# Optimization experiments

Measured on AMD Instinct MI355X. Metric: run time of the kernel, lower is better.

## Reference

```python
import jax, jax.numpy as jnp
import numpy as np

B, L, M = 512, 128, 6
ATOM_DIM, BOND_DIM, FP = 39, 10, 256


def setup_inputs() -> dict:
    key = jax.random.key(0)
    ks = jax.random.split(key, 16)
    s = 0.05
    inp = {
        'atom_list': jax.random.normal(ks[0], (B, L, ATOM_DIM), jnp.float32),
        'bond_list': jax.random.normal(ks[1], (B, L, BOND_DIM), jnp.float32),
        'atom_degree_list': jax.random.randint(ks[2], (B, L, M), 0, L),
        'bond_degree_list': jax.random.randint(ks[3], (B, L, M), 0, L),
        'atom_mask': jnp.ones((B, L), jnp.float32),
        # parameters (torch Linear convention: W [out, in], y = x @ W.T + b)
        'W_atom': jax.random.normal(ks[4], (FP, ATOM_DIM), jnp.float32) * s,
        'b_atom': jnp.zeros((FP,), jnp.float32),
        'W_nbr': jax.random.normal(ks[5], (FP, ATOM_DIM + BOND_DIM), jnp.float32) * s,
        'b_nbr': jnp.zeros((FP,), jnp.float32),
        'W_align': jax.random.normal(ks[6], (1, 2 * FP), jnp.float32) * s,
        'b_align': jnp.zeros((1,), jnp.float32),
        'W_attend': jax.random.normal(ks[7], (FP, FP), jnp.float32) * s,
        'b_attend': jnp.zeros((FP,), jnp.float32),
        # GRUCell params, gate order (r, z, n)
        'W_ih': jax.random.normal(ks[8], (3 * FP, FP), jnp.float32) * s,
        'b_ih': jnp.zeros((3 * FP,), jnp.float32),
        'W_hh': jax.random.normal(ks[9], (3 * FP, FP), jnp.float32) * s,
        'b_hh': jnp.zeros((3 * FP,), jnp.float32),
    }
    return inp


def _leaky(x):
    return jax.nn.leaky_relu(x, negative_slope=0.01)


def _gru_cell(x, h, W_ih, b_ih, W_hh, b_hh):
    gi = x @ W_ih.T + b_ih  # [N, 3F]
    gh = h @ W_hh.T + b_hh
    i_r, i_z, i_n = jnp.split(gi, 3, axis=-1)
    h_r, h_z, h_n = jnp.split(gh, 3, axis=-1)
    r = jax.nn.sigmoid(i_r + h_r)
    z = jax.nn.sigmoid(i_z + h_z)
    n = jnp.tanh(i_n + r * h_n)
    return (1.0 - z) * n + z * h


def reference(atom_list, bond_list, atom_degree_list, bond_degree_list, atom_mask,
              W_atom, b_atom, W_nbr, b_nbr, W_align, b_align, W_attend, b_attend,
              W_ih, b_ih, W_hh, b_hh):
    batch, mol_length, _ = atom_list.shape
    bidx = jnp.arange(batch)[:, None, None]

    atom_feature = _leaky(atom_list @ W_atom.T + b_atom)  # [B,L,F]

    # per-molecule neighbor gathers (irregular access)
    atom_neighbor = atom_list[bidx, atom_degree_list]   # [B,L,M,ATOM_DIM]
    bond_neighbor = bond_list[bidx, bond_degree_list]   # [B,L,M,BOND_DIM]
    neighbor_feature = jnp.concatenate([atom_neighbor, bond_neighbor], axis=-1)
    neighbor_feature = _leaky(neighbor_feature @ W_nbr.T + b_nbr)  # [B,L,M,F]

    pad = atom_degree_list == (mol_length - 1)
    attend_mask = jnp.where(pad, 0.0, 1.0)[..., None]          # [B,L,M,1]
    softmax_mask = jnp.where(pad, -9e8, 0.0)[..., None]        # [B,L,M,1]

    atom_feature_expand = jnp.broadcast_to(atom_feature[:, :, None, :],
                                           neighbor_feature.shape)
    feature_align = jnp.concatenate([atom_feature_expand, neighbor_feature], axis=-1)
    align_score = _leaky(feature_align @ W_align.T + b_align)  # [B,L,M,1]
    align_score = align_score + softmax_mask
    attention_weight = jax.nn.softmax(align_score, axis=-2) * attend_mask

    neighbor_transform = neighbor_feature @ W_attend.T + b_attend  # [B,L,M,F]
    context = jnp.sum(attention_weight * neighbor_transform, axis=-2)  # [B,L,F]
    context = jax.nn.elu(context)

    h = _gru_cell(context.reshape(-1, context.shape[-1]),
                  atom_feature.reshape(-1, atom_feature.shape[-1]),
                  W_ih, b_ih, W_hh, b_hh)
    atom_feature = h.reshape(batch, mol_length, -1)
    return jax.nn.relu(atom_feature)
```

## Files before the change

### kernel.cpp

```cpp
#include <hip/hip_runtime.h>
#include <hip/hip_bf16.h>
#include <math.h>

#define Bsz 512
#define Lm  128
#define Mn  6
#define AD  39
#define BDm 10
#define KN  49
#define F   256
#define TB  16
#define NR  96
#define NFP 264
#define ANP 72

#define WS_WATM 0
#define WS_WNBR 32768
#define WS_WATT 65536
#define WS_WIH  196608
#define WS_WHH  589824
#define WS_WALN 983040
#define WS_SUM  991232
#define WS_WN   1253376

typedef __attribute__((ext_vector_type(8))) short bf16x8;
typedef __attribute__((ext_vector_type(4))) float f32x4;
typedef __attribute__((ext_vector_type(4))) unsigned int u32x4;

__device__ __forceinline__ float lrelu(float x){ return x > 0.0f ? x : 0.01f*x; }
__device__ __forceinline__ float sigm(float x){ return 1.0f/(1.0f+__expf(-x)); }
__device__ __forceinline__ float ftanh(float x){
    float xc = fminf(fmaxf(x, -15.f), 15.f);
    float e  = __expf(2.0f*xc);
    return (e - 1.0f)/(e + 1.0f);
}
__device__ __forceinline__ float felu(float x){ return x > 0.f ? x : (__expf(x) - 1.0f); }

__device__ __forceinline__ unsigned short f2bfh(float f){
    __hip_bfloat16 h = __float2bfloat16(f);
    unsigned short s;
    __builtin_memcpy(&s, &h, 2);
    return s;
}
__device__ __forceinline__ unsigned int pack2bf(float lo, float hi){
    float2 f2; f2.x = lo; f2.y = hi;
    __hip_bfloat162 h2 = __float22bfloat162_rn(f2);
    unsigned int u;
    __builtin_memcpy(&u, &h2, 4);
    return u;
}
__device__ __forceinline__ float bf2f(unsigned short h){
    unsigned int u = ((unsigned int)h)<<16;
    return __builtin_bit_cast(float, u);
}

__global__ __launch_bounds__(256)
void p0_prep(const float* __restrict__ Watm, const float* __restrict__ Wnbr,
             const float* __restrict__ Watt, const float* __restrict__ Wih,
             const float* __restrict__ Whh,  const float* __restrict__ Waln,
             unsigned short* __restrict__ ws)
{
    int id = blockIdx.x*256 + threadIdx.x;
    if (id >= 968*512) return;
    int T = id >> 9, e = id & 511;
    int lane = e >> 3, j = e & 7;
    int col16 = lane & 15, kg = lane >> 4;
    float v; unsigned short* dst;
    if (T < 32) {
        int nt = T >> 1, ks = T & 1;
        int k = ks*32 + kg*8 + j;
        v = (k < AD) ? Watm[(nt*16 + col16)*AD + k] : 0.0f;
        dst = ws + (WS_WATM>>1) + (size_t)T*512 + e;
    } else if (T < 64) {
        int T2 = T - 32;
        int nt = T2 >> 1, ks = T2 & 1;
        int k = ks*32 + kg*8 + j;
        v = (k < KN) ? Wnbr[(nt*16 + col16)*KN + k] : 0.0f;
        dst = ws + (WS_WNBR>>1) + (size_t)T2*512 + e;
    } else if (T < 192) {
        int T2 = T - 64;
        int nt = T2 >> 3, ks = T2 & 7;
        v = Watt[(nt*16 + col16)*F + ks*32 + kg*8 + j];
        dst = ws + (WS_WATT>>1) + (size_t)T2*512 + e;
    } else if (T < 576) {
        int T3 = T - 192;
        int nt = T3 >> 3, ks = T3 & 7;
        v = Wih[(nt*16 + col16)*F + ks*32 + kg*8 + j];
        dst = ws + (WS_WIH>>1) + (size_t)T3*512 + e;
    } else if (T < 960) {
        int T4 = T - 576;
        int nt = T4 >> 3, ks = T4 & 7;
        v = Whh[(nt*16 + col16)*F + ks*32 + kg*8 + j];
        dst = ws + (WS_WHH>>1) + (size_t)T4*512 + e;
    } else {
        int ks = T - 960;
        v = (col16 == 0) ? Waln[F + ks*32 + kg*8 + j] : 0.0f;
        dst = ws + (WS_WALN>>1) + (size_t)ks*512 + e;
    }
    *dst = f2bfh(v);
}

#define NT2 512
__global__ __launch_bounds__(NT2, 6)
void k2_nbr(const float* __restrict__ atom, const float* __restrict__ bond,
            const int* __restrict__ adeg_g, const int* __restrict__ bdeg_g,
            const float* __restrict__ Walign, const float* __restrict__ balign,
            const float* __restrict__ batom,  const float* __restrict__ bnbr,
            const unsigned short* __restrict__ ws,
            unsigned short* __restrict__ wn_g, float* __restrict__ sumaw_g)
{
    __shared__ alignas(16) unsigned short nfl[NR*NFP];
    __shared__ float ascl[TB];
    __shared__ float nscl[NR];
    __shared__ float awl[NR];
    __shared__ int   adeg[NR];
    __shared__ int   bdeg[NR];
    unsigned short* stg = nfl;

    const int t  = threadIdx.x;
    const int g0 = blockIdx.x*TB;
    const int molbase = (g0/Lm)*Lm;
    const int w = t >> 6, lane = t & 63;
    const int col16 = lane & 15, kg = lane >> 4;

    bf16x8 batmf[2][2], bnbrf[2][2];
    #pragma unroll
    for (int j = 0; j < 2; ++j)
        #pragma unroll
        for (int ks = 0; ks < 2; ++ks) {
            batmf[j][ks] = *(const bf16x8*)&ws[(WS_WATM>>1) + (size_t)((2*w+j)*2 + ks)*512 + lane*8];
            bnbrf[j][ks] = *(const bf16x8*)&ws[(WS_WNBR>>1) + (size_t)((2*w+j)*2 + ks)*512 + lane*8];
        }

    if (t < NR) {
        adeg[t] = adeg_g[(size_t)g0*Mn + t];
        bdeg[t] = bdeg_g[(size_t)g0*Mn + t];
    }
    if (t < TB) ascl[t] = 0.f;
    __syncthreads();

    for (int i = t; i < 112*32; i += NT2) {
        int r = i >> 5, d0 = (i & 31)*2;
        float v0, v1;
        if (r < TB) {
            const float* src = atom + (size_t)(g0+r)*AD;
            v0 = (d0   < AD) ? src[d0]   : 0.f;
            v1 = (d0+1 < AD) ? src[d0+1] : 0.f;
        } else {
            int rr = r - TB;
            const float* asrc = atom + (size_t)(molbase + adeg[rr])*AD;
            const float* bsrc = bond + (size_t)(molbase + bdeg[rr])*BDm;
            int d1 = d0+1;
            v0 = (d0 < AD) ? asrc[d0] : ((d0 < KN) ? bsrc[d0-AD] : 0.f);
            v1 = (d1 < AD) ? asrc[d1] : ((d1 < KN) ? bsrc[d1-AD] : 0.f);
        }
        *(unsigned int*)&stg[r*ANP + d0] = pack2bf(v0, v1);
    }
    __syncthreads();

    {
        f32x4 acc[2];
        #pragma unroll
        for (int j = 0; j < 2; ++j) acc[j] = (f32x4){0.f,0.f,0.f,0.f};
        #pragma unroll
        for (int ks = 0; ks < 2; ++ks) {
            bf16x8 a = *(const bf16x8*)&stg[col16*ANP + ks*32 + kg*8];
            #pragma unroll
            for (int j = 0; j < 2; ++j)
                acc[j] = __builtin_amdgcn_mfma_f32_16x16x32_bf16(a, batmf[j][ks], acc[j], 0, 0, 0);
        }
        float ps[4] = {0.f,0.f,0.f,0.f};
        #pragma unroll
        for (int j = 0; j < 2; ++j) {
            const int col = (2*w+j)*16 + col16;
            const float bb  = batom[col];
            const float wal = Walign[col];
            #pragma unroll
            for (int jj = 0; jj < 4; ++jj) ps[jj] += lrelu(acc[j][jj] + bb)*wal;
        }
        #pragma unroll
        for (int jj = 0; jj < 4; ++jj) {
            float p = ps[jj];
            p += __shfl_xor(p, 1); p += __shfl_xor(p, 2);
            p += __shfl_xor(p, 4); p += __shfl_xor(p, 8);
            if (col16 == 0) atomicAdd(&ascl[kg*4 + jj], p);
        }
    }

    f32x4 acc[6][2];
    #pragma unroll
    for (int mt = 0; mt < 6; ++mt)
        #pragma unroll
        for (int j = 0; j < 2; ++j) acc[mt][j] = (f32x4){0.f,0.f,0.f,0.f};
    #pragma unroll
    for (int ks = 0; ks < 2; ++ks) {
        #pragma unroll
        for (int mt = 0; mt < 6; ++mt) {
            bf16x8 a = *(const bf16x8*)&stg[(TB + mt*16 + col16)*ANP + ks*32 + kg*8];
            #pragma unroll
            for (int j = 0; j < 2; ++j)
                acc[mt][j] = __builtin_amdgcn_mfma_f32_16x16x32_bf16(a, bnbrf[j][ks], acc[mt][j], 0, 0, 0);
        }
    }
    __syncthreads();

    #pragma unroll
    for (int mt = 0; mt < 6; ++mt)
        #pragma unroll
        for (int j = 0; j < 2; ++j) {
            const int col = (2*w+j)*16 + col16;
            const float bnb = bnbr[col];
            #pragma unroll
            for (int jj = 0; jj < 4; ++jj)
                nfl[(mt*16 + kg*4 + jj)*NFP + col] = f2bfh(lrelu(acc[mt][j][jj] + bnb));
        }
    __syncthreads();

    if (w < 6) {
        const int mt = w;
        f32x4 ns = {0.f,0.f,0.f,0.f};
        #pragma unroll
        for (int ks = 0; ks < 8; ++ks) {
            bf16x8 a = *(const bf16x8*)&nfl[(mt*16 + col16)*NFP + ks*32 + kg*8];
            bf16x8 b = *(const bf16x8*)&ws[(WS_WALN>>1) + (size_t)ks*512 + lane*8];
            ns = __builtin_amdgcn_mfma_f32_16x16x32_bf16(a, b, ns, 0, 0, 0);
        }
        if (col16 == 0) {
            #pragma unroll
            for (int jj = 0; jj < 4; ++jj) nscl[mt*16 + kg*4 + jj] = ns[jj];
        }
    }
    __syncthreads();

    if (t < TB) {
        const float ba = balign[0];
        const float as = ascl[t];
        float sc[Mn], msk[Mn];
        float mx = -1e30f;
        #pragma unroll
        for (int m = 0; m < Mn; ++m) {
            int pad = (adeg[t*Mn+m] == Lm-1);
            float s = lrelu(as + nscl[t*Mn+m] + ba) + (pad ? -9e8f : 0.0f);
            msk[m] = pad ? 0.f : 1.f;
            sc[m] = s; mx = fmaxf(mx, s);
        }
        float sum = 0.f;
        #pragma unroll
        for (int m = 0; m < Mn; ++m) { sc[m] = __expf(sc[m]-mx); sum += sc[m]; }
        const float inv = 1.0f/sum;
        float sa = 0.f;
        #pragma unroll
        for (int m = 0; m < Mn; ++m) { float v = sc[m]*inv*msk[m]; awl[t*Mn+m] = v; sa += v; }
        sumaw_g[g0 + t] = sa;
    }
    __syncthreads();

    {
        const int a = t & 15, cg = t >> 4;
        float o[8] = {0,0,0,0,0,0,0,0};
        #pragma unroll
        for (int m = 0; m < Mn; ++m) {
            const float aw = awl[a*Mn + m];
            u32x4 v = *(const u32x4*)&nfl[(a*Mn+m)*NFP + cg*8];
            o[0] += aw*__builtin_bit_cast(float, v.x<<16);
            o[1] += aw*__builtin_bit_cast(float, v.x & 0xffff0000u);
            o[2] += aw*__builtin_bit_cast(float, v.y<<16);
            o[3] += aw*__builtin_bit_cast(float, v.y & 0xffff0000u);
            o[4] += aw*__builtin_bit_cast(float, v.z<<16);
            o[5] += aw*__builtin_bit_cast(float, v.z & 0xffff0000u);
            o[6] += aw*__builtin_bit_cast(float, v.w<<16);
            o[7] += aw*__builtin_bit_cast(float, v.w & 0xffff0000u);
        }
        u32x4 pv;
        pv.x = pack2bf(o[0], o[1]);
        pv.y = pack2bf(o[2], o[3]);
        pv.z = pack2bf(o[4], o[5]);
        pv.w = pack2bf(o[6], o[7]);
        __builtin_nontemporal_store(pv, (u32x4*)&wn_g[(size_t)(g0+a)*F + cg*8]);
    }
}

#define NTK4 512
#define K4A  64
__global__ __launch_bounds__(NTK4)
void k4_gru(const unsigned short* __restrict__ ws,
            const unsigned short* __restrict__ wn_g,
            const float* __restrict__ atom,
            const float* __restrict__ sumaw_g, const float* __restrict__ batom,
            const float* __restrict__ batt,
            const float* __restrict__ bih, const float* __restrict__ bhh,
            float* __restrict__ out)
{
    __shared__ alignas(16) unsigned short wnl[K4A*NFP];
    __shared__ alignas(16) unsigned short afl[K4A*NFP];
    __shared__ alignas(16) unsigned short arowl[K4A*ANP];
    __shared__ float sumawl[K4A];
    const int t  = threadIdx.x;
    const int g0 = blockIdx.x*K4A;

    for (int i = t; i < K4A*32; i += NTK4) {
        int row = i >> 5, cg = i & 31;
        u32x4 v = __builtin_nontemporal_load((const u32x4*)&wn_g[(size_t)(g0+row)*F + cg*8]);
        *(u32x4*)&wnl[row*NFP + cg*8] = v;
    }
    for (int i = t; i < K4A*32; i += NTK4) {
        int r = i >> 5, d0 = (i & 31)*2;
        const float* src = atom + (size_t)(g0+r)*AD;
        float v0 = (d0   < AD) ? __builtin_nontemporal_load(&src[d0])   : 0.f;
        float v1 = (d0+1 < AD) ? __builtin_nontemporal_load(&src[d0+1]) : 0.f;
        *(unsigned int*)&arowl[r*ANP + d0] = pack2bf(v0, v1);
    }
    if (t < K4A) sumawl[t] = sumaw_g[g0 + t];
    __syncthreads();

    const int w = t >> 6, lane = t & 63;
    const int col16 = lane & 15, kg = lane >> 4;
    const unsigned short* wsAtm = ws + (WS_WATM>>1);
    const unsigned short* wsAtt = ws + (WS_WATT>>1);
    const unsigned short* wsIh  = ws + (WS_WIH>>1);
    const unsigned short* wsHh  = ws + (WS_WHH>>1);

    {
        f32x4 a0[4], a1[4];
        #pragma unroll
        for (int mt = 0; mt < 4; ++mt) { a0[mt] = (f32x4){0,0,0,0}; a1[mt] = (f32x4){0,0,0,0}; }
        #pragma unroll
        for (int ks = 0; ks < 2; ++ks) {
            bf16x8 b0 = *(const bf16x8*)&wsAtm[(size_t)((2*w)*2   + ks)*512 + lane*8];
            bf16x8 b1 = *(const bf16x8*)&wsAtm[(size_t)((2*w+1)*2 + ks)*512 + lane*8];
            #pragma unroll
            for (int mt = 0; mt < 4; ++mt) {
                bf16x8 a = *(const bf16x8*)&arowl[(mt*16 + col16)*ANP + ks*32 + kg*8];
                a0[mt] = __builtin_amdgcn_mfma_f32_16x16x32_bf16(a, b0, a0[mt], 0, 0, 0);
                a1[mt] = __builtin_amdgcn_mfma_f32_16x16x32_bf16(a, b1, a1[mt], 0, 0, 0);
            }
        }
        const float bb0 = batom[(2*w)*16   + col16];
        const float bb1 = batom[(2*w+1)*16 + col16];
        #pragma unroll
        for (int mt = 0; mt < 4; ++mt)
            #pragma unroll
            for (int jj = 0; jj < 4; ++jj) {
                int row = mt*16 + kg*4 + jj;
                afl[row*NFP + (2*w)*16   + col16] = f2bfh(lrelu(a0[mt][jj] + bb0));
                afl[row*NFP + (2*w+1)*16 + col16] = f2bfh(lrelu(a1[mt][jj] + bb1));
            }
    }

    f32x4 c0[4], c1[4];
    {
        const float bb0 = batt[(2*w)*16   + col16];
        const float bb1 = batt[(2*w+1)*16 + col16];
        #pragma unroll
        for (int mt = 0; mt < 4; ++mt)
            #pragma unroll
            for (int jj = 0; jj < 4; ++jj) {
                float sa = sumawl[mt*16 + kg*4 + jj];
                c0[mt][jj] = bb0*sa; c1[mt][jj] = bb1*sa;
            }
        #pragma unroll 2
        for (int ks = 0; ks < 8; ++ks) {
            bf16x8 b0 = *(const bf16x8*)&wsAtt[(size_t)((2*w)*8   + ks)*512 + lane*8];
            bf16x8 b1 = *(const bf16x8*)&wsAtt[(size_t)((2*w+1)*8 + ks)*512 + lane*8];
            #pragma unroll
            for (int mt = 0; mt < 4; ++mt) {
                bf16x8 a = *(const bf16x8*)&wnl[(mt*16 + col16)*NFP + ks*32 + kg*8];
                c0[mt] = __builtin_amdgcn_mfma_f32_16x16x32_bf16(a, b0, c0[mt], 0, 0, 0);
                c1[mt] = __builtin_amdgcn_mfma_f32_16x16x32_bf16(a, b1, c1[mt], 0, 0, 0);
            }
        }
    }
    __syncthreads();
    unsigned short* ctxl = wnl;
    #pragma unroll
    for (int mt = 0; mt < 4; ++mt)
        #pragma unroll
        for (int jj = 0; jj < 4; ++jj) {
            int row = mt*16 + kg*4 + jj;
            ctxl[row*NFP + (2*w)*16   + col16] = f2bfh(felu(c0[mt][jj]));
            ctxl[row*NFP + (2*w+1)*16 + col16] = f2bfh(felu(c1[mt][jj]));
        }
    __syncthreads();

    #pragma unroll 1
    for (int q = 0; q < 2; ++q) {
        const int nt0 = 2*w + q;
        const int f   = w*32 + q*16 + col16;
        f32x4 rA[4], zA[4], nA[4], hA[4];
        {
            const float rb = bih[f]     + bhh[f];
            const float zb = bih[F+f]   + bhh[F+f];
            const float nb = bih[2*F+f];
            const float hb = bhh[2*F+f];
            #pragma unroll
            for (int mt = 0; mt < 4; ++mt)
                #pragma unroll
                for (int jj = 0; jj < 4; ++jj) {
                    rA[mt][jj] = rb; zA[mt][jj] = zb;
                    nA[mt][jj] = nb; hA[mt][jj] = hb;
                }
        }
        #pragma unroll 1
        for (int ks = 0; ks < 8; ++ks) {
            bf16x8 bir = *(const bf16x8*)&wsIh[(size_t)(( 0 + nt0)*8 + ks)*512 + lane*8];
            bf16x8 bhr = *(const bf16x8*)&wsHh[(size_t)(( 0 + nt0)*8 + ks)*512 + lane*8];
            bf16x8 biz = *(const bf16x8*)&wsIh[(size_t)((16 + nt0)*8 + ks)*512 + lane*8];
            bf16x8 bhz = *(const bf16x8*)&wsHh[(size_t)((16 + nt0)*8 + ks)*512 + lane*8];
            bf16x8 bin = *(const bf16x8*)&wsIh[(size_t)((32 + nt0)*8 + ks)*512 + lane*8];
            bf16x8 bhn = *(const bf16x8*)&wsHh[(size_t)((32 + nt0)*8 + ks)*512 + lane*8];
            #pragma unroll
            for (int mt = 0; mt < 4; ++mt) {
                bf16x8 ac = *(const bf16x8*)&ctxl[(mt*16 + col16)*NFP + ks*32 + kg*8];
                bf16x8 ah = *(const bf16x8*)&afl [(mt*16 + col16)*NFP + ks*32 + kg*8];
                rA[mt] = __builtin_amdgcn_mfma_f32_16x16x32_bf16(ac, bir, rA[mt], 0, 0, 0);
                rA[mt] = __builtin_amdgcn_mfma_f32_16x16x32_bf16(ah, bhr, rA[mt], 0, 0, 0);
                zA[mt] = __builtin_amdgcn_mfma_f32_16x16x32_bf16(ac, biz, zA[mt], 0, 0, 0);
                zA[mt] = __builtin_amdgcn_mfma_f32_16x16x32_bf16(ah, bhz, zA[mt], 0, 0, 0);
                nA[mt] = __builtin_amdgcn_mfma_f32_16x16x32_bf16(ac, bin, nA[mt], 0, 0, 0);
                hA[mt] = __builtin_amdgcn_mfma_f32_16x16x32_bf16(ah, bhn, hA[mt], 0, 0, 0);
            }
        }
        #pragma unroll
        for (int mt = 0; mt < 4; ++mt)
            #pragma unroll
            for (int jj = 0; jj < 4; ++jj) {
                int a = mt*16 + kg*4 + jj;
                float r = sigm(rA[mt][jj]);
                float z = sigm(zA[mt][jj]);
                float n = ftanh(nA[mt][jj] + r*hA[mt][jj]);
                float h = bf2f(afl[a*NFP + f]);
                float o = (1.f - z)*n + z*h;
                __builtin_nontemporal_store(fmaxf(o, 0.f), &out[(size_t)(g0+a)*F + f]);
            }
    }
}

extern "C" void kernel_launch(void* const* d_in, const int* in_sizes, int n_in,
                              void* d_out, int out_size, void* d_ws, size_t ws_size,
                              hipStream_t stream) {
    const float* atom_list = (const float*)d_in[0];
    const float* bond_list = (const float*)d_in[1];
    const int*   adeg      = (const int*)  d_in[2];
    const int*   bdeg      = (const int*)  d_in[3];
    const float* W_atom  = (const float*)d_in[5];
    const float* b_atom  = (const float*)d_in[6];
    const float* W_nbr   = (const float*)d_in[7];
    const float* b_nbr   = (const float*)d_in[8];
    const float* W_align = (const float*)d_in[9];
    const float* b_align = (const float*)d_in[10];
    const float* W_att   = (const float*)d_in[11];
    const float* b_att   = (const float*)d_in[12];
    const float* W_ih    = (const float*)d_in[13];
    const float* b_ih    = (const float*)d_in[14];
    const float* W_hh    = (const float*)d_in[15];
    const float* b_hh    = (const float*)d_in[16];
    float* out = (float*)d_out;

    unsigned short* wsu = (unsigned short*)d_ws;
    float* sumaw        = (float*)((char*)d_ws + WS_SUM);
    unsigned short* wn  = (unsigned short*)((char*)d_ws + WS_WN);

    p0_prep<<<1936, 256, 0, stream>>>(W_atom, W_nbr, W_att, W_ih, W_hh, W_align, wsu);
    k2_nbr<<<(Bsz*Lm)/TB, NT2, 0, stream>>>(atom_list, bond_list, adeg, bdeg,
                                            W_align, b_align, b_atom, b_nbr,
                                            wsu, wn, sumaw);
    k4_gru<<<(Bsz*Lm)/K4A, NTK4, 0, stream>>>(wsu, wn, atom_list, sumaw,
                                              b_atom, b_att, b_ih, b_hh, out);
}
```

Measured before the change: 177.6 us.

## Reuse k2 atom features in GRU kernel via workspace and swizzle LDS

k2 already computes the atom-feature projection for its tile. It now writes the activated result to a bf16 workspace buffer, and k4 loads it instead of recomputing W_atom from the raw atom rows. This removes k4's atom-row staging and its extra MFMA stage, at the cost of an extra 32MB global write and read round trip. k4's shared buffers also drop the row padding and use an XOR swizzle to avoid bank conflicts, which shrinks LDS use and may raise occupancy.

```diff
diff --git a/kernel.cpp b/kernel.cpp
--- a/kernel.cpp
+++ b/kernel.cpp
@@ -13,6 +13,7 @@
 #define NR  96
 #define NFP 264
 #define ANP 72
+#define NF2 256
 
 #define WS_WATM 0
 #define WS_WNBR 32768
@@ -21,7 +22,8 @@
 #define WS_WHH  589824
 #define WS_WALN 983040
 #define WS_SUM  991232
-#define WS_WN   1253376
+#define WS_AF   1253376
+#define WS_WN   34807808
 
 typedef __attribute__((ext_vector_type(8))) short bf16x8;
 typedef __attribute__((ext_vector_type(4))) float f32x4;
@@ -52,6 +54,9 @@
 __device__ __forceinline__ float bf2f(unsigned short h){
     unsigned int u = ((unsigned int)h)<<16;
     return __builtin_bit_cast(float, u);
+}
+__device__ __forceinline__ int swz(int row, int col){
+    return row*NF2 + (col ^ ((row & 7) << 3));
 }
 
 __global__ __launch_bounds__(256)
@@ -107,6 +112,7 @@
             const float* __restrict__ Walign, const float* __restrict__ balign,
             const float* __restrict__ batom,  const float* __restrict__ bnbr,
             const unsigned short* __restrict__ ws,
+            unsigned short* __restrict__ af_g,
             unsigned short* __restrict__ wn_g, float* __restrict__ sumaw_g)
 {
     __shared__ alignas(16) unsigned short nfl[NR*NFP];
@@ -176,7 +182,11 @@
             const float bb  = batom[col];
             const float wal = Walign[col];
             #pragma unroll
-            for (int jj = 0; jj < 4; ++jj) ps[jj] += lrelu(acc[j][jj] + bb)*wal;
+            for (int jj = 0; jj < 4; ++jj) {
+                float v = lrelu(acc[j][jj] + bb);
+                __builtin_nontemporal_store(f2bfh(v), &af_g[(size_t)(g0 + kg*4 + jj)*F + col]);
+                ps[jj] += v*wal;
+            }
         }
         #pragma unroll
         for (int jj = 0; jj < 4; ++jj) {
@@ -285,67 +295,35 @@
 __global__ __launch_bounds__(NTK4)
 void k4_gru(const unsigned short* __restrict__ ws,
             const unsigned short* __restrict__ wn_g,
-            const float* __restrict__ atom,
-            const float* __restrict__ sumaw_g, const float* __restrict__ batom,
+            const unsigned short* __restrict__ af_g,
+            const float* __restrict__ sumaw_g,
             const float* __restrict__ batt,
             const float* __restrict__ bih, const float* __restrict__ bhh,
             float* __restrict__ out)
 {
-    __shared__ alignas(16) unsigned short wnl[K4A*NFP];
-    __shared__ alignas(16) unsigned short afl[K4A*NFP];
-    __shared__ alignas(16) unsigned short arowl[K4A*ANP];
+    __shared__ alignas(16) unsigned short wnl[K4A*NF2];
+    __shared__ alignas(16) unsigned short afl[K4A*NF2];
     __shared__ float sumawl[K4A];
     const int t  = threadIdx.x;
     const int g0 = blockIdx.x*K4A;
 
-    for (int i = t; i < K4A*32; i += NTK4) {
-        int row = i >> 5, cg = i & 31;
-        u32x4 v = __builtin_nontemporal_load((const u32x4*)&wn_g[(size_t)(g0+row)*F + cg*8]);
-        *(u32x4*)&wnl[row*NFP + cg*8] = v;
-    }
-    for (int i = t; i < K4A*32; i += NTK4) {
-        int r = i >> 5, d0 = (i & 31)*2;
-        const float* src = atom + (size_t)(g0+r)*AD;
-        float v0 = (d0   < AD) ? __builtin_nontemporal_load(&src[d0])   : 0.f;
-        float v1 = (d0+1 < AD) ? __builtin_nontemporal_load(&src[d0+1]) : 0.f;
-        *(unsigned int*)&arowl[r*ANP + d0] = pack2bf(v0, v1);
+    for (int i = t; i < K4A*32*2; i += NTK4) {
+        int m = i >> 11;
+        int ii = i & 2047;
+        int row = ii >> 5, cg = ii & 31;
+        const unsigned short* src = m ? af_g : wn_g;
+        unsigned short* dst = m ? afl : wnl;
+        u32x4 v = __builtin_nontemporal_load((const u32x4*)&src[(size_t)(g0+row)*F + cg*8]);
+        *(u32x4*)&dst[swz(row, cg*8)] = v;
     }
     if (t < K4A) sumawl[t] = sumaw_g[g0 + t];
     __syncthreads();
 
     const int w = t >> 6, lane = t & 63;
     const int col16 = lane & 15, kg = lane >> 4;
-    const unsigned short* wsAtm = ws + (WS_WATM>>1);
     const unsigned short* wsAtt = ws + (WS_WATT>>1);
     const unsigned short* wsIh  = ws + (WS_WIH>>1);
     const unsigned short* wsHh  = ws + (WS_WHH>>1);
-
-    {
-        f32x4 a0[4], a1[4];
-        #pragma unroll
-        for (int mt = 0; mt < 4; ++mt) { a0[mt] = (f32x4){0,0,0,0}; a1[mt] = (f32x4){0,0,0,0}; }
-        #pragma unroll
-        for (int ks = 0; ks < 2; ++ks) {
-            bf16x8 b0 = *(const bf16x8*)&wsAtm[(size_t)((2*w)*2   + ks)*512 + lane*8];
-            bf16x8 b1 = *(const bf16x8*)&wsAtm[(size_t)((2*w+1)*2 + ks)*512 + lane*8];
-            #pragma unroll
-            for (int mt = 0; mt < 4; ++mt) {
-                bf16x8 a = *(const bf16x8*)&arowl[(mt*16 + col16)*ANP + ks*32 + kg*8];
-                a0[mt] = __builtin_amdgcn_mfma_f32_16x16x32_bf16(a, b0, a0[mt], 0, 0, 0);
-                a1[mt] = __builtin_amdgcn_mfma_f32_16x16x32_bf16(a, b1, a1[mt], 0, 0, 0);
-            }
-        }
-        const float bb0 = batom[(2*w)*16   + col16];
-        const float bb1 = batom[(2*w+1)*16 + col16];
-        #pragma unroll
-        for (int mt = 0; mt < 4; ++mt)
-            #pragma unroll
-            for (int jj = 0; jj < 4; ++jj) {
-                int row = mt*16 + kg*4 + jj;
-                afl[row*NFP + (2*w)*16   + col16] = f2bfh(lrelu(a0[mt][jj] + bb0));
-                afl[row*NFP + (2*w+1)*16 + col16] = f2bfh(lrelu(a1[mt][jj] + bb1));
-            }
-    }
 
     f32x4 c0[4], c1[4];
     {
@@ -364,7 +342,7 @@
             bf16x8 b1 = *(const bf16x8*)&wsAtt[(size_t)((2*w+1)*8 + ks)*512 + lane*8];
             #pragma unroll
             for (int mt = 0; mt < 4; ++mt) {
-                bf16x8 a = *(const bf16x8*)&wnl[(mt*16 + col16)*NFP + ks*32 + kg*8];
+                bf16x8 a = *(const bf16x8*)&wnl[swz(mt*16 + col16, ks*32 + kg*8)];
                 c0[mt] = __builtin_amdgcn_mfma_f32_16x16x32_bf16(a, b0, c0[mt], 0, 0, 0);
                 c1[mt] = __builtin_amdgcn_mfma_f32_16x16x32_bf16(a, b1, c1[mt], 0, 0, 0);
             }
@@ -377,8 +355,8 @@
         #pragma unroll
         for (int jj = 0; jj < 4; ++jj) {
             int row = mt*16 + kg*4 + jj;
-            ctxl[row*NFP + (2*w)*16   + col16] = f2bfh(felu(c0[mt][jj]));
-            ctxl[row*NFP + (2*w+1)*16 + col16] = f2bfh(felu(c1[mt][jj]));
+            ctxl[swz(row, (2*w)*16   + col16)] = f2bfh(felu(c0[mt][jj]));
+            ctxl[swz(row, (2*w+1)*16 + col16)] = f2bfh(felu(c1[mt][jj]));
         }
     __syncthreads();
 
@@ -410,8 +388,8 @@
             bf16x8 bhn = *(const bf16x8*)&wsHh[(size_t)((32 + nt0)*8 + ks)*512 + lane*8];
             #pragma unroll
             for (int mt = 0; mt < 4; ++mt) {
-                bf16x8 ac = *(const bf16x8*)&ctxl[(mt*16 + col16)*NFP + ks*32 + kg*8];
-                bf16x8 ah = *(const bf16x8*)&afl [(mt*16 + col16)*NFP + ks*32 + kg*8];
+                bf16x8 ac = *(const bf16x8*)&ctxl[swz(mt*16 + col16, ks*32 + kg*8)];
+                bf16x8 ah = *(const bf16x8*)&afl [swz(mt*16 + col16, ks*32 + kg*8)];
                 rA[mt] = __builtin_amdgcn_mfma_f32_16x16x32_bf16(ac, bir, rA[mt], 0, 0, 0);
                 rA[mt] = __builtin_amdgcn_mfma_f32_16x16x32_bf16(ah, bhr, rA[mt], 0, 0, 0);
                 zA[mt] = __builtin_amdgcn_mfma_f32_16x16x32_bf16(ac, biz, zA[mt], 0, 0, 0);
@@ -428,7 +406,7 @@
                 float r = sigm(rA[mt][jj]);
                 float z = sigm(zA[mt][jj]);
                 float n = ftanh(nA[mt][jj] + r*hA[mt][jj]);
-                float h = bf2f(afl[a*NFP + f]);
+                float h = bf2f(afl[swz(a, f)]);
                 float o = (1.f - z)*n + z*h;
                 __builtin_nontemporal_store(fmaxf(o, 0.f), &out[(size_t)(g0+a)*F + f]);
             }
@@ -456,14 +434,15 @@
     const float* b_hh    = (const float*)d_in[16];
     float* out = (float*)d_out;
 
-    unsigned short* wsu = (unsigned short*)d_ws;
-    float* sumaw        = (float*)((char*)d_ws + WS_SUM);
-    unsigned short* wn  = (unsigned short*)((char*)d_ws + WS_WN);
+    unsigned short* wsu   = (unsigned short*)d_ws;
+    float* sumaw          = (float*)((char*)d_ws + WS_SUM);
+    unsigned short* af_bf = (unsigned short*)((char*)d_ws + WS_AF);
+    unsigned short* wn    = (unsigned short*)((char*)d_ws + WS_WN);
 
     p0_prep<<<1936, 256, 0, stream>>>(W_atom, W_nbr, W_att, W_ih, W_hh, W_align, wsu);
     k2_nbr<<<(Bsz*Lm)/TB, NT2, 0, stream>>>(atom_list, bond_list, adeg, bdeg,
                                             W_align, b_align, b_atom, b_nbr,
-                                            wsu, wn, sumaw);
-    k4_gru<<<(Bsz*Lm)/K4A, NTK4, 0, stream>>>(wsu, wn, atom_list, sumaw,
-                                              b_atom, b_att, b_ih, b_hh, out);
-}
+                                            wsu, af_bf, wn, sumaw);
+    k4_gru<<<(Bsz*Lm)/K4A, NTK4, 0, stream>>>(wsu, wn, af_bf, sumaw,
+                                              b_att, b_ih, b_hh, out);
+}
```

Result: no change. 178.4 us (+0.5%).
